# Kernel tuning notes

Measured on AMD Instinct MI355X. Metric: run time of the kernel, lower is better.

Reference implementation:

```python
import jax, jax.numpy as jnp
import numpy as np

B, T, D, U = 64, 512, 1024, 1024


def hard_sigmoid(x):
    # keras hard_sigmoid: clip(0.2*x + 0.5, 0, 1)
    return jnp.clip(0.2 * x + 0.5, 0.0, 1.0)


def setup_inputs() -> dict:
    key = jax.random.key(0)
    ks = jax.random.split(key, 6)
    x = jax.random.normal(ks[0], (B, T, D), jnp.float32)
    # glorot-ish scaled params
    kernel = jax.random.normal(ks[1], (D, 4 * U), jnp.float32) * (1.0 / np.sqrt(D).astype(np.float32))
    recurrent_kernel = jax.random.normal(ks[2], (U, 4 * U), jnp.float32) * (1.0 / np.sqrt(U).astype(np.float32))
    peephole_kernel = jax.random.normal(ks[3], (U, 3 * U), jnp.float32) * (1.0 / np.sqrt(U).astype(np.float32))
    projection_kernel = jax.random.normal(ks[4], (U, U), jnp.float32) * (1.0 / np.sqrt(U).astype(np.float32))
    # unit_forget_bias: [zeros(U), ones(U), zeros(2U)] for (i, f, c, o)
    bias = jnp.concatenate([jnp.zeros((U,), jnp.float32), jnp.ones((U,), jnp.float32), jnp.zeros((2 * U,), jnp.float32)])
    h0 = jnp.zeros((B, U), jnp.float32)
    c0 = jnp.zeros((B, U), jnp.float32)
    return {"x": x, "h0": h0, "c0": c0, "kernel": kernel, "recurrent_kernel": recurrent_kernel,
            "peephole_kernel": peephole_kernel, "projection_kernel": projection_kernel, "bias": bias}


def reference(x, h0, c0, kernel, recurrent_kernel, peephole_kernel, projection_kernel, bias):
    U_ = h0.shape[-1]
    Pi = peephole_kernel[:, :U_]
    Pf = peephole_kernel[:, U_:2 * U_]
    Po = peephole_kernel[:, 2 * U_:3 * U_]

    def step(carry, x_t):
        h, c = carry
        # fused gate pre-activations: [B, 4U]
        z = x_t @ kernel + h @ recurrent_kernel + bias
        zi, zf, zc, zo = jnp.split(z, 4, axis=-1)
        i = hard_sigmoid(zi + c @ Pi)            # input gate w/ peephole on c_{t-1}
        f = hard_sigmoid(zf + c @ Pf)            # forget gate w/ peephole on c_{t-1}
        c_new = f * c + i * jnp.tanh(zc)
        o = hard_sigmoid(zo + c_new @ Po)        # output gate w/ peephole on c_t
        # residual LSTM: project tanh(c_t), add residual input, gate by o
        h_new = o * (jnp.tanh(c_new) @ projection_kernel + x_t)
        return (h_new, c_new), h_new

    xs = jnp.swapaxes(x, 0, 1)  # [T, B, D]
    (_, _), hs = jax.lax.scan(step, (h0, c0), xs)
    return jnp.swapaxes(hs, 0, 1)  # [B, T, U]
```

## Files before the change

### kernel.cpp

```cpp
#include <hip/hip_runtime.h>
#include <cstdint>
#include <cstddef>

#define NB 64
#define NT 512
#define ND 1024
#define NU 1024

typedef short s16x8 __attribute__((ext_vector_type(8)));
typedef float f32x4 __attribute__((ext_vector_type(4)));
typedef unsigned int u32x2 __attribute__((ext_vector_type(2)));
typedef unsigned int u32x4 __attribute__((ext_vector_type(4)));
typedef unsigned short u16;

__device__ __forceinline__ u16 f2bf(float f) {
  unsigned int u = __float_as_uint(f);
  u += 0x7fffu + ((u >> 16) & 1u);
  return (u16)(u >> 16);
}
__device__ __forceinline__ float bf2f(u16 s) {
  return __uint_as_float(((unsigned int)s) << 16);
}
__device__ __forceinline__ float hsig(float x) {
  return fminf(fmaxf(0.2f * x + 0.5f, 0.0f), 1.0f);
}
__device__ __forceinline__ float ftanh(float x) {
  float e = __expf(2.0f * x);
  return 1.0f - 2.0f / (e + 1.0f);
}
__device__ __forceinline__ f32x4 mfma16(s16x8 a, s16x8 b, f32x4 c) {
  return __builtin_amdgcn_mfma_f32_16x16x32_bf16(a, b, c, 0, 0, 0);
}

__device__ __forceinline__ void atomic_swap_u32(unsigned int* p, unsigned int v) {
  asm volatile("global_atomic_swap %0, %1, off" :: "v"(p), "v"(v) : "memory");
}
__device__ __forceinline__ void atomic_swap_u64(unsigned int* p, u32x2 v) {
  asm volatile("global_atomic_swap_x2 %0, %1, off" :: "v"(p), "v"(v) : "memory");
}

template <int STAGED>
__device__ __forceinline__ void ldx4(s16x8& d, const u16* a) {
  if constexpr (STAGED)
    asm volatile("global_load_dwordx4 %0, %1, off" : "=v"(d) : "v"(a));
  else
    asm volatile("global_load_dwordx4 %0, %1, off sc0 sc1" : "=v"(d) : "v"(a));
}

#define WAIT_VM0() do { \
    asm volatile("s_waitcnt vmcnt(0)" ::: "memory"); \
    __builtin_amdgcn_sched_barrier(0); \
  } while (0)
#define WAIT_VM(N) do { \
    asm volatile("s_waitcnt vmcnt(" #N ")" ::: "memory"); \
    __builtin_amdgcn_sched_barrier(0); \
  } while (0)

__global__ __launch_bounds__(256) void wt_cvt(const float* __restrict__ W,
                                              u16* __restrict__ Wt) {
  __shared__ u16 T[64][65];
  const int tid = threadIdx.x;
  const int k0 = (blockIdx.x & 15) * 64;
  const int n0 = (blockIdx.x >> 4) * 64;
  const int r = tid >> 2, c4 = (tid & 3) * 16;
  {
    const float* src = W + (size_t)(k0 + r) * 4096 + n0 + c4;
#pragma unroll
    for (int j = 0; j < 4; ++j) {
      float4 v = ((const float4*)src)[j];
      T[r][c4 + j * 4 + 0] = f2bf(v.x); T[r][c4 + j * 4 + 1] = f2bf(v.y);
      T[r][c4 + j * 4 + 2] = f2bf(v.z); T[r][c4 + j * 4 + 3] = f2bf(v.w);
    }
  }
  __syncthreads();
  {
    u16 tmp[16];
#pragma unroll
    for (int i = 0; i < 16; ++i) tmp[i] = T[c4 + i][r];
    u16* dst = Wt + (size_t)(n0 + r) * 1024 + k0 + c4;
    *(s16x8*)dst = *(s16x8*)tmp;
    *(s16x8*)(dst + 8) = *(s16x8*)(tmp + 8);
  }
}

template <int WT>
__global__ __launch_bounds__(256) void xw_gemm(const float* __restrict__ X,
                                               const float* __restrict__ W,
                                               const u16* __restrict__ Wt,
                                               u16* __restrict__ XW) {
  __shared__ u16 Al[128][72];
  __shared__ u16 Bl[128][72];
  const int tid = threadIdx.x;
  const int lane = tid & 63;
  const int wv = tid >> 6;
  const int m0 = (blockIdx.x >> 5) * 128;
  const int n0 = (blockIdx.x & 31) * 128;
  f32x4 acc[4][4];
#pragma unroll
  for (int i = 0; i < 4; ++i)
#pragma unroll
    for (int j = 0; j < 4; ++j) acc[i][j] = (f32x4){0.f, 0.f, 0.f, 0.f};

  for (int kt = 0; kt < 1024; kt += 64) {
    {
      const int r = tid >> 1, hh = (tid & 1) * 32;
      const float* src = X + (size_t)(m0 + r) * 1024 + kt + hh;
      u16* dst = &Al[r][hh];
      if constexpr (WT) {
#pragma unroll
        for (int j = 0; j < 4; ++j) {
          float4 v0 = ((const float4*)src)[2 * j];
          float4 v1 = ((const float4*)src)[2 * j + 1];
          u32x4 q;
          q[0] = ((unsigned)f2bf(v0.y) << 16) | f2bf(v0.x);
          q[1] = ((unsigned)f2bf(v0.w) << 16) | f2bf(v0.z);
          q[2] = ((unsigned)f2bf(v1.y) << 16) | f2bf(v1.x);
          q[3] = ((unsigned)f2bf(v1.w) << 16) | f2bf(v1.z);
          *(u32x4*)(dst + j * 8) = q;
        }
      } else {
#pragma unroll
        for (int j = 0; j < 8; ++j) {
          float4 v = ((const float4*)src)[j];
          dst[j * 4 + 0] = f2bf(v.x); dst[j * 4 + 1] = f2bf(v.y);
          dst[j * 4 + 2] = f2bf(v.z); dst[j * 4 + 3] = f2bf(v.w);
        }
      }
    }
    if constexpr (WT) {
      const int n = tid >> 1, kh = (tid & 1) * 32;
      const u16* src = Wt + (size_t)(n0 + n) * 1024 + kt + kh;
      u16* dst = &Bl[n][kh];
#pragma unroll
      for (int j = 0; j < 4; ++j)
        *(s16x8*)(dst + j * 8) = *(const s16x8*)(src + j * 8);
    } else {
      const int kr = tid >> 2, q = (tid & 3) * 32;
      const float* src = W + (size_t)(kt + kr) * 4096 + n0 + q;
#pragma unroll
      for (int j = 0; j < 8; ++j) {
        float4 v = ((const float4*)src)[j];
        const int n = q + j * 4;
        Bl[n + 0][kr] = f2bf(v.x); Bl[n + 1][kr] = f2bf(v.y);
        Bl[n + 2][kr] = f2bf(v.z); Bl[n + 3][kr] = f2bf(v.w);
      }
    }
    __syncthreads();
    const int wm = (wv >> 1) * 64, wn = (wv & 1) * 64;
    const int row = lane & 15, kq = (lane >> 4) * 8;
#pragma unroll
    for (int ks = 0; ks < 2; ++ks) {
      s16x8 af[4], bq[4];
#pragma unroll
      for (int i = 0; i < 4; ++i) af[i] = *(const s16x8*)&Al[wm + i * 16 + row][ks * 32 + kq];
#pragma unroll
      for (int j = 0; j < 4; ++j) bq[j] = *(const s16x8*)&Bl[wn + j * 16 + row][ks * 32 + kq];
#pragma unroll
      for (int i = 0; i < 4; ++i)
#pragma unroll
        for (int j = 0; j < 4; ++j) acc[i][j] = mfma16(af[i], bq[j], acc[i][j]);
    }
    __syncthreads();
  }
  const int wm = (wv >> 1) * 64, wn = (wv & 1) * 64;
  const int col16 = lane & 15, rq = (lane >> 4) * 4;
#pragma unroll
  for (int i = 0; i < 4; ++i)
#pragma unroll
    for (int j = 0; j < 4; ++j)
#pragma unroll
      for (int q = 0; q < 4; ++q) {
        const int m = m0 + wm + i * 16 + rq + q;
        const int n = n0 + wn + j * 16 + col16;
        const int t = m & 511, b = m >> 9;
        const int g = n >> 10, uu = n & 1023;
        const int ugrp = uu >> 4, ul2 = uu & 15;
        XW[(((size_t)ugrp * 512 + t) * 64 + b) * 64 + ul2 * 4 + g] = f2bf(acc[i][j][q]);
      }
}

__global__ void init_comm(const float* __restrict__ h0, const float* __restrict__ c0,
                          u16* hini, u16* cini) {
  const int i = blockIdx.x * 256 + threadIdx.x;
  hini[i] = f2bf(h0[i]);
  cini[i] = f2bf(c0[i]);
}

__device__ __forceinline__ void gbar_arrive(unsigned int* flags, int bid, int tid,
                                            unsigned int ep) {
  __syncthreads();
  if (tid == 0) atomic_swap_u32(flags + bid * 16, ep);
}
__device__ __forceinline__ void gbar_poll(unsigned int* flags, int rq, int tid,
                                          unsigned int ep) {
  unsigned int* f = flags + ((((tid & 63) << 2) | rq) * 16);
  for (;;) {
    unsigned int v;
    asm volatile("global_load_dword %0, %1, off sc0 sc1\n\ts_waitcnt vmcnt(0)"
                 : "=v"(v) : "v"(f) : "memory");
    if (v >= ep) break;
    __builtin_amdgcn_s_sleep(1);
  }
  __builtin_amdgcn_sched_barrier(0);
}

#define WLDS_B   (64 * 1032 * 2)
#define ZOFF     WLDS_B
#define POFF     (ZOFF + 16 * 68 * 4)
#define OOFF     (POFF + 16 * 36 * 4)
#define SMEM_B   (OOFF + 16 * 36 * 4)
#define STEP_E   65536

template <int STAGED>
__global__ __launch_bounds__(256, 1) void lstm_loop(
    const float* __restrict__ rec, const float* __restrict__ peep,
    const float* __restrict__ projw, const float* __restrict__ bias,
    const float* __restrict__ x, const u16* __restrict__ xw,
    float* __restrict__ out,
    u16* hini, u16* cini, u16* cb0, u16* cb1, u16* thsg,
    u16* hst, u16* cst, u16* thst,
    unsigned int* flags, const float* __restrict__ c0) {
  extern __shared__ char smem[];
  u16 (*wlds)[1032] = (u16(*)[1032])smem;
  float (*zlds)[68] = (float(*)[68])(smem + ZOFF);
  float (*plds)[36] = (float(*)[36])(smem + POFF);
  float (*olds)[36] = (float(*)[36])(smem + OOFF);

  const int tid = threadIdx.x;
  const int lane = tid & 63;
  const int wv = tid >> 6;
  const int bid = blockIdx.x;
  const int ugrp = bid >> 2;
  const int rq = bid & 3;
  const int row0 = rq * 16;
  const int u0 = ugrp * 16;
  const int fcol = lane & 15;
  const int kofs = (lane >> 4) * 8;

  for (int g = 0; g < 8; ++g) {
    const int c = g * 8 + (tid & 3) * 2;
    const int scol = (c >> 4) * 1024 + u0 + (c & 15);
#pragma unroll 4
    for (int p = 0; p < 16; ++p) {
      const int k = p * 64 + (tid >> 2);
      float2 v = *(const float2*)(rec + (size_t)k * 4096 + scol);
      wlds[c][k] = f2bf(v.x);
      wlds[c + 1][k] = f2bf(v.y);
    }
  }
  __syncthreads();
  s16x8 breg[32];
#pragma unroll
  for (int kt = 0; kt < 32; ++kt)
    breg[kt] = *(const s16x8*)&wlds[wv * 16 + fcol][kt * 32 + kofs];
  __syncthreads();
  for (int g = 0; g < 8; ++g) {
    const int c = g * 8 + (tid & 3) * 2;
    const float* sp; int stride, scol;
    if (c < 48) { sp = peep;  stride = 3072; scol = (c >> 4) * 1024 + u0 + (c & 15); }
    else        { sp = projw; stride = 1024; scol = u0 + (c & 15); }
#pragma unroll 4
    for (int p = 0; p < 16; ++p) {
      const int k = p * 64 + (tid >> 2);
      float2 v = *(const float2*)(sp + (size_t)k * stride + scol);
      wlds[c][k] = f2bf(v.x);
      wlds[c + 1][k] = f2bf(v.y);
    }
  }

  const int r = tid >> 4;
  const int ul = tid & 15;
  const int brow = row0 + r;
  const int u = u0 + ul;
  const float b_i = bias[u], b_f = bias[1024 + u], b_c = bias[2048 + u], b_o = bias[3072 + u];
  float cstv = c0[brow * 1024 + u];

  u32x2 xwp;
  float xp;
  {
    const u16* xr0 = xw + (((size_t)ugrp * 512 + 0) * 64 + brow) * 64 + ul * 4;
    asm volatile("global_load_dwordx2 %0, %1, off" : "=v"(xwp) : "v"(xr0));
    const float* xs0 = x + (size_t)brow * (512 * 1024) + u;
    asm volatile("global_load_dword %0, %1, off" : "=v"(xp) : "v"(xs0));
  }
  __syncthreads();

  for (int t = 0; t < NT; ++t) {
    const size_t xo = (size_t)brow * (512 * 1024) + (size_t)t * 1024 + u;
    float zo_reg, xres, hv;

    const u16 *hsrc, *cpsrc, *csrc, *thsrc; u16 *cpub, *thpub, *hpub;
    if constexpr (STAGED) {
      hsrc  = t ? (hst + (size_t)(t - 1) * STEP_E) : hini;
      cpsrc = t ? (cst + (size_t)(t - 1) * STEP_E) : cini;
      cpub  = cst + (size_t)t * STEP_E;   csrc = cpub;
      thpub = thst + (size_t)t * STEP_E;  thsrc = thpub;
      hpub  = hst + (size_t)t * STEP_E;
    } else {
      hsrc = hini; hpub = hini;
      cpub = (t & 1) ? cb1 : cb0; csrc = cpub;
      cpsrc = (t == 0) ? cini : ((t & 1) ? cb0 : cb1);
      thpub = thsg; thsrc = thsg;
    }

    s16x8 av[32];
    if (wv < 2) {
      s16x8 cv[32];
      {
        const u16* ap = cpsrc + (size_t)(row0 + fcol) * 1024 + kofs;
#pragma unroll
        for (int kt = 0; kt < 32; ++kt) ldx4<STAGED>(cv[kt], ap + kt * 32);
      }
      gbar_poll(flags, rq, tid, 2 * (unsigned)t);
      f32x4 accP = {0.f, 0.f, 0.f, 0.f};
      const u16* bp = &wlds[wv * 16 + fcol][kofs];
#pragma unroll
      for (int kt = 0; kt < 32; ++kt)
        accP = mfma16(cv[kt], *(const s16x8*)(bp + kt * 32), accP);
      {
        const u16* ap = hsrc + (size_t)(row0 + fcol) * 1024 + kofs;
#pragma unroll
        for (int kt = 0; kt < 32; ++kt) ldx4<STAGED>(av[kt], ap + kt * 32);
      }
      WAIT_VM0();
      f32x4 accZ = {0.f, 0.f, 0.f, 0.f};
#pragma unroll
      for (int kt = 0; kt < 32; ++kt) accZ = mfma16(av[kt], breg[kt], accZ);
      const int srow = (lane >> 4) * 4;
#pragma unroll
      for (int q = 0; q < 4; ++q) {
        zlds[srow + q][wv * 16 + fcol] = accZ[q];
        plds[srow + q][wv * 16 + fcol] = accP[q];
      }
    } else {
      gbar_poll(flags, rq, tid, 2 * (unsigned)t);
      {
        const u16* ap = hsrc + (size_t)(row0 + fcol) * 1024 + kofs;
#pragma unroll
        for (int kt = 0; kt < 32; ++kt) ldx4<STAGED>(av[kt], ap + kt * 32);
      }
      WAIT_VM0();
      f32x4 accZ = {0.f, 0.f, 0.f, 0.f};
#pragma unroll
      for (int kt = 0; kt < 32; ++kt) accZ = mfma16(av[kt], breg[kt], accZ);
      const int srow = (lane >> 4) * 4;
#pragma unroll
      for (int q = 0; q < 4; ++q) zlds[srow + q][wv * 16 + fcol] = accZ[q];
    }
    __syncthreads();
    {
      const float xw_i = bf2f((u16)(xwp[0] & 0xffffu));
      const float xw_f = bf2f((u16)(xwp[0] >> 16));
      const float xw_c = bf2f((u16)(xwp[1] & 0xffffu));
      const float xw_o = bf2f((u16)(xwp[1] >> 16));
      xres = xp;
      const float zi = zlds[r][ul]      + xw_i + b_i + plds[r][ul];
      const float zf = zlds[r][16 + ul] + xw_f + b_f + plds[r][16 + ul];
      const float zc = zlds[r][32 + ul] + xw_c + b_c;
      zo_reg         = zlds[r][48 + ul] + xw_o + b_o;
      const float ig = hsig(zi), fg = hsig(zf);
      cstv = fg * cstv + ig * ftanh(zc);
      const float th = ftanh(cstv);
      const unsigned int cb = f2bf(cstv), tb = f2bf(th);
      const unsigned int cp = ((unsigned)__shfl_xor((int)cb, 1) << 16) | cb;
      const unsigned int tp = ((unsigned)__shfl_xor((int)tb, 1) << 16) | tb;
      const unsigned int cp2 = (unsigned)__shfl_xor((int)cp, 2);
      const unsigned int tp2 = (unsigned)__shfl_xor((int)tp, 2);
      if ((ul & 3) == 0) {
        u32x2 cq; cq[0] = cp; cq[1] = cp2;
        u32x2 tq; tq[0] = tp; tq[1] = tp2;
        atomic_swap_u64((unsigned int*)(cpub + brow * 1024 + u), cq);
        atomic_swap_u64((unsigned int*)(thpub + brow * 1024 + u), tq);
      }
    }
    WAIT_VM0();
    gbar_arrive(flags, bid, tid, 2 * t + 1);

    if (!STAGED || wv >= 2) gbar_poll(flags, rq, tid, 2 * t + 1);
    if (wv >= 2) {
      const u16* ap = ((wv == 2) ? csrc : thsrc)
                      + (size_t)(row0 + fcol) * 1024 + kofs;
#pragma unroll
      for (int kt = 0; kt < 32; ++kt) ldx4<STAGED>(av[kt], ap + kt * 32);
      WAIT_VM0();
      f32x4 acc = {0.f, 0.f, 0.f, 0.f};
      const u16* bp = &wlds[wv * 16 + fcol][kofs];
#pragma unroll
      for (int kt = 0; kt < 32; ++kt)
        acc = mfma16(av[kt], *(const s16x8*)(bp + kt * 32), acc);
      const int srow = (lane >> 4) * 4;
#pragma unroll
      for (int q = 0; q < 4; ++q) olds[srow + q][(wv - 2) * 16 + fcol] = acc[q];
    }
    __syncthreads();
    {
      const float og = hsig(zo_reg + olds[r][ul]);
      const float pv = olds[r][16 + ul] + xres;
      hv = og * pv;
      const unsigned int hb = f2bf(hv);
      const unsigned int hp = ((unsigned)__shfl_xor((int)hb, 1) << 16) | hb;
      const unsigned int hp2 = (unsigned)__shfl_xor((int)hp, 2);
      if ((ul & 3) == 0) {
        u32x2 hq; hq[0] = hp; hq[1] = hp2;
        atomic_swap_u64((unsigned int*)(hpub + brow * 1024 + u), hq);
      }
      const int tn = (t + 1 < NT) ? (t + 1) : t;
      const u16* xrn = xw + (((size_t)ugrp * 512 + tn) * 64 + brow) * 64 + ul * 4;
      asm volatile("global_load_dwordx2 %0, %1, off" : "=v"(xwp) : "v"(xrn));
      const float* xsn = x + (size_t)brow * (512 * 1024) + (size_t)tn * 1024 + u;
      asm volatile("global_load_dword %0, %1, off" : "=v"(xp) : "v"(xsn));
      asm volatile("global_store_dword %0, %1, off" :: "v"(out + xo), "v"(hv) : "memory");
      WAIT_VM(3);
    }
    gbar_arrive(flags, bid, tid, 2 * t + 2);
  }
}

extern "C" void kernel_launch(void* const* d_in, const int* in_sizes, int n_in,
                              void* d_out, int out_size, void* d_ws, size_t ws_size,
                              hipStream_t stream) {
  const float* x    = (const float*)d_in[0];
  const float* h0   = (const float*)d_in[1];
  const float* c0   = (const float*)d_in[2];
  const float* W    = (const float*)d_in[3];
  const float* R    = (const float*)d_in[4];
  const float* P    = (const float*)d_in[5];
  const float* PRJ  = (const float*)d_in[6];
  const float* bias = (const float*)d_in[7];
  float* out = (float*)d_out;
  char* ws = (char*)d_ws;

  const size_t XW_BYTES = (size_t)32768 * 4096 * 2;
  size_t off = XW_BYTES;
  u16* xw   = (u16*)ws;
  u16* hini = (u16*)(ws + off); off += 131072;
  u16* cini = (u16*)(ws + off); off += 131072;
  u16* cb0  = (u16*)(ws + off); off += 131072;
  u16* cb1  = (u16*)(ws + off); off += 131072;
  u16* thsg = (u16*)(ws + off); off += 131072;
  unsigned int* flags = (unsigned int*)(ws + off); off += 16384;
  const size_t base_need = off;
  u16* hst = (u16*)(ws + off);  off += (size_t)NT * 131072;
  u16* cst = (u16*)(ws + off);  off += (size_t)NT * 131072;
  u16* thst = (u16*)(ws + off); off += (size_t)NT * 131072;
  const size_t staged_need = off;
  u16* Wt = (u16*)(ws + off); off += (size_t)4096 * 1024 * 2;
  const size_t wt_need = off;
  if (ws_size < base_need) return;
  const int staged = (ws_size >= staged_need) ? 1 : 0;
  const int wt = (ws_size >= wt_need) ? 1 : 0;

  (void)hipFuncSetAttribute(reinterpret_cast<const void*>(&lstm_loop<1>),
                            hipFuncAttributeMaxDynamicSharedMemorySize, 160 * 1024);
  (void)hipFuncSetAttribute(reinterpret_cast<const void*>(&lstm_loop<0>),
                            hipFuncAttributeMaxDynamicSharedMemorySize, 160 * 1024);

  hipMemsetAsync(flags, 0, 16384, stream);
  hipLaunchKernelGGL(init_comm, dim3(256), dim3(256), 0, stream, h0, c0, hini, cini);
  if (wt) {
    hipLaunchKernelGGL(wt_cvt, dim3(1024), dim3(256), 0, stream, W, Wt);
    hipLaunchKernelGGL((xw_gemm<1>), dim3(8192), dim3(256), 0, stream, x, W, Wt, xw);
  } else {
    hipLaunchKernelGGL((xw_gemm<0>), dim3(8192), dim3(256), 0, stream, x, W, Wt, xw);
  }

  void* args[17];
  args[0] = (void*)&R;     args[1] = (void*)&P;     args[2] = (void*)&PRJ;
  args[3] = (void*)&bias;  args[4] = (void*)&x;     args[5] = (void*)&xw;
  args[6] = (void*)&out;   args[7] = (void*)&hini;  args[8] = (void*)&cini;
  args[9] = (void*)&cb0;   args[10] = (void*)&cb1;  args[11] = (void*)&thsg;
  args[12] = (void*)&hst;  args[13] = (void*)&cst;  args[14] = (void*)&thst;
  args[15] = (void*)&flags; args[16] = (void*)&c0;

  const void* fn = staged ? (const void*)&lstm_loop<1> : (const void*)&lstm_loop<0>;
  hipError_t e = hipLaunchCooperativeKernel(fn, dim3(256), dim3(256),
                                            args, (unsigned int)SMEM_B, stream);
  if (e != hipSuccess) {
    if (staged)
      hipLaunchKernelGGL((lstm_loop<1>), dim3(256), dim3(256), SMEM_B, stream,
                         R, P, PRJ, bias, x, xw, out, hini, cini, cb0, cb1, thsg,
                         hst, cst, thst, flags, c0);
    else
      hipLaunchKernelGGL((lstm_loop<0>), dim3(256), dim3(256), SMEM_B, stream,
                         R, P, PRJ, bias, x, xw, out, hini, cini, cb0, cb1, thsg,
                         hst, cst, thst, flags, c0);
  }
}
```

Measured before the change: 7.169 ms.

## Poll barrier flags per k-slice group and overlap loads with partial arrivals

Replaces the all-flags barrier poll with per-16-lane-group polling. Each quarter of the K dimension is loaded and multiplied as soon as the producer blocks owning that slice have arrived, so waiting overlaps with MFMA work instead of stalling on the slowest producer. The peephole c-matmul now runs fully before the h-poll, and wave 0-1 no longer polls the second epoch in the non-staged path. The risk is more poll round-trips per step, shorter load batches with a full vmcnt wait per slice, and possible ordering bugs if a group's flag coverage does not match its k-slice.

Result: slower. 7.542 ms (+5.2%).

```diff
diff --git a/kernel.cpp b/kernel.cpp
--- a/kernel.cpp
+++ b/kernel.cpp
@@ -191,18 +191,62 @@
   __syncthreads();
   if (tid == 0) atomic_swap_u32(flags + bid * 16, ep);
 }
-__device__ __forceinline__ void gbar_poll(unsigned int* flags, int rq, int tid,
-                                          unsigned int ep) {
-  unsigned int* f = flags + ((((tid & 63) << 2) | rq) * 16);
-  for (;;) {
-    unsigned int v;
-    asm volatile("global_load_dword %0, %1, off sc0 sc1\n\ts_waitcnt vmcnt(0)"
-                 : "=v"(v) : "v"(f) : "memory");
-    if (v >= ep) break;
-    __builtin_amdgcn_s_sleep(1);
-  }
-  __builtin_amdgcn_sched_barrier(0);
-}
+
+#define POLL_GRP(S, EP) \
+  do { \
+    if ((lane >> 4) == (S)) { \
+      unsigned int pv_; \
+      for (;;) { \
+        asm volatile("global_load_dword %0, %1, off sc0 sc1\n\ts_waitcnt vmcnt(0)" \
+                     : "=v"(pv_) : "v"(myflag) : "memory"); \
+        if (pv_ >= (EP)) break; \
+        __builtin_amdgcn_s_sleep(1); \
+      } \
+    } \
+    __builtin_amdgcn_sched_barrier(0); \
+  } while (0)
+
+#define ZCONS(S) do { \
+    s16x8 a0_, a1_, a2_, a3_, a4_, a5_, a6_, a7_; \
+    ldx4<STAGED>(a0_, ap + ((S) * 8 + 0) * 32); \
+    ldx4<STAGED>(a1_, ap + ((S) * 8 + 1) * 32); \
+    ldx4<STAGED>(a2_, ap + ((S) * 8 + 2) * 32); \
+    ldx4<STAGED>(a3_, ap + ((S) * 8 + 3) * 32); \
+    ldx4<STAGED>(a4_, ap + ((S) * 8 + 4) * 32); \
+    ldx4<STAGED>(a5_, ap + ((S) * 8 + 5) * 32); \
+    ldx4<STAGED>(a6_, ap + ((S) * 8 + 6) * 32); \
+    ldx4<STAGED>(a7_, ap + ((S) * 8 + 7) * 32); \
+    WAIT_VM0(); \
+    accZ = mfma16(a0_, breg[(S) * 8 + 0], accZ); \
+    accZ = mfma16(a1_, breg[(S) * 8 + 1], accZ); \
+    accZ = mfma16(a2_, breg[(S) * 8 + 2], accZ); \
+    accZ = mfma16(a3_, breg[(S) * 8 + 3], accZ); \
+    accZ = mfma16(a4_, breg[(S) * 8 + 4], accZ); \
+    accZ = mfma16(a5_, breg[(S) * 8 + 5], accZ); \
+    accZ = mfma16(a6_, breg[(S) * 8 + 6], accZ); \
+    accZ = mfma16(a7_, breg[(S) * 8 + 7], accZ); \
+  } while (0)
+
+#define OCONS(S) do { \
+    s16x8 a0_, a1_, a2_, a3_, a4_, a5_, a6_, a7_; \
+    ldx4<STAGED>(a0_, ap2 + ((S) * 8 + 0) * 32); \
+    ldx4<STAGED>(a1_, ap2 + ((S) * 8 + 1) * 32); \
+    ldx4<STAGED>(a2_, ap2 + ((S) * 8 + 2) * 32); \
+    ldx4<STAGED>(a3_, ap2 + ((S) * 8 + 3) * 32); \
+    ldx4<STAGED>(a4_, ap2 + ((S) * 8 + 4) * 32); \
+    ldx4<STAGED>(a5_, ap2 + ((S) * 8 + 5) * 32); \
+    ldx4<STAGED>(a6_, ap2 + ((S) * 8 + 6) * 32); \
+    ldx4<STAGED>(a7_, ap2 + ((S) * 8 + 7) * 32); \
+    WAIT_VM0(); \
+    accO = mfma16(a0_, *(const s16x8*)(bp2 + ((S) * 8 + 0) * 32), accO); \
+    accO = mfma16(a1_, *(const s16x8*)(bp2 + ((S) * 8 + 1) * 32), accO); \
+    accO = mfma16(a2_, *(const s16x8*)(bp2 + ((S) * 8 + 2) * 32), accO); \
+    accO = mfma16(a3_, *(const s16x8*)(bp2 + ((S) * 8 + 3) * 32), accO); \
+    accO = mfma16(a4_, *(const s16x8*)(bp2 + ((S) * 8 + 4) * 32), accO); \
+    accO = mfma16(a5_, *(const s16x8*)(bp2 + ((S) * 8 + 5) * 32), accO); \
+    accO = mfma16(a6_, *(const s16x8*)(bp2 + ((S) * 8 + 6) * 32), accO); \
+    accO = mfma16(a7_, *(const s16x8*)(bp2 + ((S) * 8 + 7) * 32), accO); \
+  } while (0)
 
 #define WLDS_B   (64 * 1032 * 2)
 #define ZOFF     WLDS_B
@@ -275,6 +319,8 @@
   const float b_i = bias[u], b_f = bias[1024 + u], b_c = bias[2048 + u], b_o = bias[3072 + u];
   float cstv = c0[brow * 1024 + u];
 
+  unsigned int* myflag = flags + (((lane << 2) | rq) * 16);
+
   u32x2 xwp;
   float xp;
   {
@@ -303,46 +349,29 @@
       thpub = thsg; thsrc = thsg;
     }
 
-    s16x8 av[32];
     if (wv < 2) {
       s16x8 cv[32];
-      {
-        const u16* ap = cpsrc + (size_t)(row0 + fcol) * 1024 + kofs;
-#pragma unroll
-        for (int kt = 0; kt < 32; ++kt) ldx4<STAGED>(cv[kt], ap + kt * 32);
-      }
-      gbar_poll(flags, rq, tid, 2 * (unsigned)t);
+      const u16* cap = cpsrc + (size_t)(row0 + fcol) * 1024 + kofs;
+#pragma unroll
+      for (int kt = 0; kt < 32; ++kt) ldx4<STAGED>(cv[kt], cap + kt * 32);
+      WAIT_VM0();
       f32x4 accP = {0.f, 0.f, 0.f, 0.f};
-      const u16* bp = &wlds[wv * 16 + fcol][kofs];
+      const u16* pbp = &wlds[wv * 16 + fcol][kofs];
 #pragma unroll
       for (int kt = 0; kt < 32; ++kt)
-        accP = mfma16(cv[kt], *(const s16x8*)(bp + kt * 32), accP);
-      {
-        const u16* ap = hsrc + (size_t)(row0 + fcol) * 1024 + kofs;
-#pragma unroll
-        for (int kt = 0; kt < 32; ++kt) ldx4<STAGED>(av[kt], ap + kt * 32);
-      }
-      WAIT_VM0();
+        accP = mfma16(cv[kt], *(const s16x8*)(pbp + kt * 32), accP);
+      const int srow = (lane >> 4) * 4;
+#pragma unroll
+      for (int q = 0; q < 4; ++q) plds[srow + q][wv * 16 + fcol] = accP[q];
+    }
+    {
+      const unsigned int ep1 = 2 * (unsigned)t;
+      const u16* ap = hsrc + (size_t)(row0 + fcol) * 1024 + kofs;
       f32x4 accZ = {0.f, 0.f, 0.f, 0.f};
-#pragma unroll
-      for (int kt = 0; kt < 32; ++kt) accZ = mfma16(av[kt], breg[kt], accZ);
-      const int srow = (lane >> 4) * 4;
-#pragma unroll
-      for (int q = 0; q < 4; ++q) {
-        zlds[srow + q][wv * 16 + fcol] = accZ[q];
-        plds[srow + q][wv * 16 + fcol] = accP[q];
-      }
-    } else {
-      gbar_poll(flags, rq, tid, 2 * (unsigned)t);
-      {
-        const u16* ap = hsrc + (size_t)(row0 + fcol) * 1024 + kofs;
-#pragma unroll
-        for (int kt = 0; kt < 32; ++kt) ldx4<STAGED>(av[kt], ap + kt * 32);
-      }
-      WAIT_VM0();
-      f32x4 accZ = {0.f, 0.f, 0.f, 0.f};
-#pragma unroll
-      for (int kt = 0; kt < 32; ++kt) accZ = mfma16(av[kt], breg[kt], accZ);
+      POLL_GRP(0, ep1); ZCONS(0);
+      POLL_GRP(1, ep1); ZCONS(1);
+      POLL_GRP(2, ep1); ZCONS(2);
+      POLL_GRP(3, ep1); ZCONS(3);
       const int srow = (lane >> 4) * 4;
 #pragma unroll
       for (int q = 0; q < 4; ++q) zlds[srow + q][wv * 16 + fcol] = accZ[q];
@@ -376,21 +405,19 @@
     WAIT_VM0();
     gbar_arrive(flags, bid, tid, 2 * t + 1);
 
-    if (!STAGED || wv >= 2) gbar_poll(flags, rq, tid, 2 * t + 1);
     if (wv >= 2) {
-      const u16* ap = ((wv == 2) ? csrc : thsrc)
-                      + (size_t)(row0 + fcol) * 1024 + kofs;
-#pragma unroll
-      for (int kt = 0; kt < 32; ++kt) ldx4<STAGED>(av[kt], ap + kt * 32);
-      WAIT_VM0();
-      f32x4 acc = {0.f, 0.f, 0.f, 0.f};
-      const u16* bp = &wlds[wv * 16 + fcol][kofs];
-#pragma unroll
-      for (int kt = 0; kt < 32; ++kt)
-        acc = mfma16(av[kt], *(const s16x8*)(bp + kt * 32), acc);
+      const unsigned int ep2 = 2 * (unsigned)t + 1;
+      const u16* ap2 = ((wv == 2) ? csrc : thsrc)
+                       + (size_t)(row0 + fcol) * 1024 + kofs;
+      const u16* bp2 = &wlds[wv * 16 + fcol][kofs];
+      f32x4 accO = {0.f, 0.f, 0.f, 0.f};
+      POLL_GRP(0, ep2); OCONS(0);
+      POLL_GRP(1, ep2); OCONS(1);
+      POLL_GRP(2, ep2); OCONS(2);
+      POLL_GRP(3, ep2); OCONS(3);
       const int srow = (lane >> 4) * 4;
 #pragma unroll
-      for (int q = 0; q < 4; ++q) olds[srow + q][(wv - 2) * 16 + fcol] = acc[q];
+      for (int q = 0; q < 4; ++q) olds[srow + q][(wv - 2) * 16 + fcol] = accO[q];
     }
     __syncthreads();
     {
```

## Replace flag-based grid barriers with epoch-tagged data words polled directly

Applied to the files above, without the earlier changes.

Removes the global flag barriers between timesteps. Each published h, c and tanh(c) element now goes into a 32-bit word whose upper 16 bits carry the step epoch, in double-buffered slots. Consumers spin-load the data itself until every word carries the expected epoch, then pack the bf16 halves for MFMA. This drops the barrier round trips and the separate flag polling, but it doubles the communication bytes, adds unpack ALU work, and relies on per-word atomic visibility for correctness.

Result: slower. 13.36 ms (+86.3%).

```diff
diff --git a/kernel.cpp b/kernel.cpp
--- a/kernel.cpp
+++ b/kernel.cpp
@@ -32,27 +32,15 @@
   return __builtin_amdgcn_mfma_f32_16x16x32_bf16(a, b, c, 0, 0, 0);
 }
 
-__device__ __forceinline__ void atomic_swap_u32(unsigned int* p, unsigned int v) {
-  asm volatile("global_atomic_swap %0, %1, off" :: "v"(p), "v"(v) : "memory");
-}
 __device__ __forceinline__ void atomic_swap_u64(unsigned int* p, u32x2 v) {
   asm volatile("global_atomic_swap_x2 %0, %1, off" :: "v"(p), "v"(v) : "memory");
 }
-
-template <int STAGED>
-__device__ __forceinline__ void ldx4(s16x8& d, const u16* a) {
-  if constexpr (STAGED)
-    asm volatile("global_load_dwordx4 %0, %1, off" : "=v"(d) : "v"(a));
-  else
-    asm volatile("global_load_dwordx4 %0, %1, off sc0 sc1" : "=v"(d) : "v"(a));
+__device__ __forceinline__ void ldw4(u32x4& d, const unsigned int* a) {
+  asm volatile("global_load_dwordx4 %0, %1, off sc0 sc1" : "=v"(d) : "v"(a));
 }
 
 #define WAIT_VM0() do { \
     asm volatile("s_waitcnt vmcnt(0)" ::: "memory"); \
-    __builtin_amdgcn_sched_barrier(0); \
-  } while (0)
-#define WAIT_VM(N) do { \
-    asm volatile("s_waitcnt vmcnt(" #N ")" ::: "memory"); \
     __builtin_amdgcn_sched_barrier(0); \
   } while (0)
 
@@ -180,28 +168,41 @@
 }
 
 __global__ void init_comm(const float* __restrict__ h0, const float* __restrict__ c0,
-                          u16* hini, u16* cini) {
+                          unsigned int* h2, unsigned int* c2) {
   const int i = blockIdx.x * 256 + threadIdx.x;
-  hini[i] = f2bf(h0[i]);
-  cini[i] = f2bf(c0[i]);
-}
-
-__device__ __forceinline__ void gbar_arrive(unsigned int* flags, int bid, int tid,
-                                            unsigned int ep) {
-  __syncthreads();
-  if (tid == 0) atomic_swap_u32(flags + bid * 16, ep);
-}
-__device__ __forceinline__ void gbar_poll(unsigned int* flags, int rq, int tid,
-                                          unsigned int ep) {
-  unsigned int* f = flags + ((((tid & 63) << 2) | rq) * 16);
-  for (;;) {
-    unsigned int v;
-    asm volatile("global_load_dword %0, %1, off sc0 sc1\n\ts_waitcnt vmcnt(0)"
-                 : "=v"(v) : "v"(f) : "memory");
-    if (v >= ep) break;
-    __builtin_amdgcn_s_sleep(1);
-  }
-  __builtin_amdgcn_sched_barrier(0);
+  h2[65536 + i] = (unsigned int)f2bf(h0[i]);
+  c2[65536 + i] = (unsigned int)f2bf(c0[i]);
+}
+
+__device__ __forceinline__ f32x4 consume_lds(const unsigned int* ap, const u16* bp,
+                                             unsigned int ep, f32x4 acc) {
+#pragma unroll
+  for (int ch = 0; ch < 4; ++ch) {
+    u32x4 w[16];
+    for (;;) {
+#pragma unroll
+      for (int j = 0; j < 16; ++j)
+        ldw4(w[j], ap + ch * 256 + (j >> 1) * 32 + (j & 1) * 4);
+      WAIT_VM0();
+      bool ok = true;
+#pragma unroll
+      for (int j = 0; j < 16; ++j)
+#pragma unroll
+        for (int e = 0; e < 4; ++e) ok = ok && ((w[j][e] >> 16) == ep);
+      if (__all(ok)) break;
+      __builtin_amdgcn_s_sleep(1);
+    }
+#pragma unroll
+    for (int i = 0; i < 8; ++i) {
+      u32x4 p;
+      p[0] = (w[2 * i][1] << 16) | (w[2 * i][0] & 0xffffu);
+      p[1] = (w[2 * i][3] << 16) | (w[2 * i][2] & 0xffffu);
+      p[2] = (w[2 * i + 1][1] << 16) | (w[2 * i + 1][0] & 0xffffu);
+      p[3] = (w[2 * i + 1][3] << 16) | (w[2 * i + 1][2] & 0xffffu);
+      acc = mfma16(*(const s16x8*)&p, *(const s16x8*)(bp + (ch * 8 + i) * 32), acc);
+    }
+  }
+  return acc;
 }
 
 #define WLDS_B   (64 * 1032 * 2)
@@ -209,17 +210,15 @@
 #define POFF     (ZOFF + 16 * 68 * 4)
 #define OOFF     (POFF + 16 * 36 * 4)
 #define SMEM_B   (OOFF + 16 * 36 * 4)
-#define STEP_E   65536
-
-template <int STAGED>
+#define SLOT_W   65536u
+
 __global__ __launch_bounds__(256, 1) void lstm_loop(
     const float* __restrict__ rec, const float* __restrict__ peep,
     const float* __restrict__ projw, const float* __restrict__ bias,
     const float* __restrict__ x, const u16* __restrict__ xw,
     float* __restrict__ out,
-    u16* hini, u16* cini, u16* cb0, u16* cb1, u16* thsg,
-    u16* hst, u16* cst, u16* thst,
-    unsigned int* flags, const float* __restrict__ c0) {
+    unsigned int* h2, unsigned int* c2, unsigned int* th2,
+    const float* __restrict__ c0) {
   extern __shared__ char smem[];
   u16 (*wlds)[1032] = (u16(*)[1032])smem;
   float (*zlds)[68] = (float(*)[68])(smem + ZOFF);
@@ -285,64 +284,53 @@
   }
   __syncthreads();
 
+  const size_t lrow = (size_t)(row0 + fcol) * 1024 + kofs;
+  const size_t prow = (size_t)brow * 1024 + u;
+
   for (int t = 0; t < NT; ++t) {
     const size_t xo = (size_t)brow * (512 * 1024) + (size_t)t * 1024 + u;
+    const unsigned int sPrev = ((unsigned)(t + 1) & 1u) * SLOT_W;
+    const unsigned int sCur  = ((unsigned)t & 1u) * SLOT_W;
+    const unsigned int epPrev = (unsigned)t;
+    const unsigned int epCur  = (unsigned)(t + 1);
     float zo_reg, xres, hv;
 
-    const u16 *hsrc, *cpsrc, *csrc, *thsrc; u16 *cpub, *thpub, *hpub;
-    if constexpr (STAGED) {
-      hsrc  = t ? (hst + (size_t)(t - 1) * STEP_E) : hini;
-      cpsrc = t ? (cst + (size_t)(t - 1) * STEP_E) : cini;
-      cpub  = cst + (size_t)t * STEP_E;   csrc = cpub;
-      thpub = thst + (size_t)t * STEP_E;  thsrc = thpub;
-      hpub  = hst + (size_t)t * STEP_E;
-    } else {
-      hsrc = hini; hpub = hini;
-      cpub = (t & 1) ? cb1 : cb0; csrc = cpub;
-      cpsrc = (t == 0) ? cini : ((t & 1) ? cb0 : cb1);
-      thpub = thsg; thsrc = thsg;
-    }
-
-    s16x8 av[32];
     if (wv < 2) {
-      s16x8 cv[32];
-      {
-        const u16* ap = cpsrc + (size_t)(row0 + fcol) * 1024 + kofs;
-#pragma unroll
-        for (int kt = 0; kt < 32; ++kt) ldx4<STAGED>(cv[kt], ap + kt * 32);
-      }
-      gbar_poll(flags, rq, tid, 2 * (unsigned)t);
-      f32x4 accP = {0.f, 0.f, 0.f, 0.f};
-      const u16* bp = &wlds[wv * 16 + fcol][kofs];
-#pragma unroll
-      for (int kt = 0; kt < 32; ++kt)
-        accP = mfma16(cv[kt], *(const s16x8*)(bp + kt * 32), accP);
-      {
-        const u16* ap = hsrc + (size_t)(row0 + fcol) * 1024 + kofs;
-#pragma unroll
-        for (int kt = 0; kt < 32; ++kt) ldx4<STAGED>(av[kt], ap + kt * 32);
-      }
-      WAIT_VM0();
+      f32x4 accP = consume_lds(c2 + sPrev + lrow, &wlds[wv * 16 + fcol][kofs],
+                               epPrev, (f32x4){0.f, 0.f, 0.f, 0.f});
+      const int srow = (lane >> 4) * 4;
+#pragma unroll
+      for (int q = 0; q < 4; ++q) plds[srow + q][wv * 16 + fcol] = accP[q];
+    }
+    {
+      const unsigned int* hp = h2 + sPrev + lrow;
       f32x4 accZ = {0.f, 0.f, 0.f, 0.f};
 #pragma unroll
-      for (int kt = 0; kt < 32; ++kt) accZ = mfma16(av[kt], breg[kt], accZ);
-      const int srow = (lane >> 4) * 4;
-#pragma unroll
-      for (int q = 0; q < 4; ++q) {
-        zlds[srow + q][wv * 16 + fcol] = accZ[q];
-        plds[srow + q][wv * 16 + fcol] = accP[q];
-      }
-    } else {
-      gbar_poll(flags, rq, tid, 2 * (unsigned)t);
-      {
-        const u16* ap = hsrc + (size_t)(row0 + fcol) * 1024 + kofs;
-#pragma unroll
-        for (int kt = 0; kt < 32; ++kt) ldx4<STAGED>(av[kt], ap + kt * 32);
-      }
-      WAIT_VM0();
-      f32x4 accZ = {0.f, 0.f, 0.f, 0.f};
-#pragma unroll
-      for (int kt = 0; kt < 32; ++kt) accZ = mfma16(av[kt], breg[kt], accZ);
+      for (int ch = 0; ch < 4; ++ch) {
+        u32x4 w[16];
+        for (;;) {
+#pragma unroll
+          for (int j = 0; j < 16; ++j)
+            ldw4(w[j], hp + ch * 256 + (j >> 1) * 32 + (j & 1) * 4);
+          WAIT_VM0();
+          bool ok = true;
+#pragma unroll
+          for (int j = 0; j < 16; ++j)
+#pragma unroll
+            for (int e = 0; e < 4; ++e) ok = ok && ((w[j][e] >> 16) == epPrev);
+          if (__all(ok)) break;
+          __builtin_amdgcn_s_sleep(1);
+        }
+#pragma unroll
+        for (int i = 0; i < 8; ++i) {
+          u32x4 p;
+          p[0] = (w[2 * i][1] << 16) | (w[2 * i][0] & 0xffffu);
+          p[1] = (w[2 * i][3] << 16) | (w[2 * i][2] & 0xffffu);
+          p[2] = (w[2 * i + 1][1] << 16) | (w[2 * i + 1][0] & 0xffffu);
+          p[3] = (w[2 * i + 1][3] << 16) | (w[2 * i + 1][2] & 0xffffu);
+          accZ = mfma16(*(const s16x8*)&p, breg[ch * 8 + i], accZ);
+        }
+      }
       const int srow = (lane >> 4) * 4;
 #pragma unroll
       for (int q = 0; q < 4; ++q) zlds[srow + q][wv * 16 + fcol] = accZ[q];
@@ -361,48 +349,37 @@
       const float ig = hsig(zi), fg = hsig(zf);
       cstv = fg * cstv + ig * ftanh(zc);
       const float th = ftanh(cstv);
-      const unsigned int cb = f2bf(cstv), tb = f2bf(th);
-      const unsigned int cp = ((unsigned)__shfl_xor((int)cb, 1) << 16) | cb;
-      const unsigned int tp = ((unsigned)__shfl_xor((int)tb, 1) << 16) | tb;
-      const unsigned int cp2 = (unsigned)__shfl_xor((int)cp, 2);
-      const unsigned int tp2 = (unsigned)__shfl_xor((int)tp, 2);
-      if ((ul & 3) == 0) {
-        u32x2 cq; cq[0] = cp; cq[1] = cp2;
-        u32x2 tq; tq[0] = tp; tq[1] = tp2;
-        atomic_swap_u64((unsigned int*)(cpub + brow * 1024 + u), cq);
-        atomic_swap_u64((unsigned int*)(thpub + brow * 1024 + u), tq);
-      }
-    }
-    WAIT_VM0();
-    gbar_arrive(flags, bid, tid, 2 * t + 1);
-
-    if (!STAGED || wv >= 2) gbar_poll(flags, rq, tid, 2 * t + 1);
+      const unsigned int epw = epCur << 16;
+      const unsigned int wc = epw | f2bf(cstv);
+      const unsigned int wt_ = epw | f2bf(th);
+      const unsigned int wc1 = (unsigned)__shfl_xor((int)wc, 1);
+      const unsigned int wt1 = (unsigned)__shfl_xor((int)wt_, 1);
+      if ((ul & 1) == 0) {
+        u32x2 cq; cq[0] = wc;  cq[1] = wc1;
+        u32x2 tq; tq[0] = wt_; tq[1] = wt1;
+        atomic_swap_u64(c2 + sCur + prow, cq);
+        atomic_swap_u64(th2 + sCur + prow, tq);
+      }
+    }
+
     if (wv >= 2) {
-      const u16* ap = ((wv == 2) ? csrc : thsrc)
-                      + (size_t)(row0 + fcol) * 1024 + kofs;
-#pragma unroll
-      for (int kt = 0; kt < 32; ++kt) ldx4<STAGED>(av[kt], ap + kt * 32);
-      WAIT_VM0();
-      f32x4 acc = {0.f, 0.f, 0.f, 0.f};
-      const u16* bp = &wlds[wv * 16 + fcol][kofs];
-#pragma unroll
-      for (int kt = 0; kt < 32; ++kt)
-        acc = mfma16(av[kt], *(const s16x8*)(bp + kt * 32), acc);
+      const unsigned int* ap2 = ((wv == 2) ? c2 : th2) + sCur + lrow;
+      f32x4 accO = consume_lds(ap2, &wlds[wv * 16 + fcol][kofs],
+                               epCur, (f32x4){0.f, 0.f, 0.f, 0.f});
       const int srow = (lane >> 4) * 4;
 #pragma unroll
-      for (int q = 0; q < 4; ++q) olds[srow + q][(wv - 2) * 16 + fcol] = acc[q];
+      for (int q = 0; q < 4; ++q) olds[srow + q][(wv - 2) * 16 + fcol] = accO[q];
     }
     __syncthreads();
     {
       const float og = hsig(zo_reg + olds[r][ul]);
       const float pv = olds[r][16 + ul] + xres;
       hv = og * pv;
-      const unsigned int hb = f2bf(hv);
-      const unsigned int hp = ((unsigned)__shfl_xor((int)hb, 1) << 16) | hb;
-      const unsigned int hp2 = (unsigned)__shfl_xor((int)hp, 2);
-      if ((ul & 3) == 0) {
-        u32x2 hq; hq[0] = hp; hq[1] = hp2;
-        atomic_swap_u64((unsigned int*)(hpub + brow * 1024 + u), hq);
+      const unsigned int hw = (epCur << 16) | f2bf(hv);
+      const unsigned int hw1 = (unsigned)__shfl_xor((int)hw, 1);
+      if ((ul & 1) == 0) {
+        u32x2 hq; hq[0] = hw; hq[1] = hw1;
+        atomic_swap_u64(h2 + sCur + prow, hq);
       }
       const int tn = (t + 1 < NT) ? (t + 1) : t;
       const u16* xrn = xw + (((size_t)ugrp * 512 + tn) * 64 + brow) * 64 + ul * 4;
@@ -410,10 +387,9 @@
       const float* xsn = x + (size_t)brow * (512 * 1024) + (size_t)tn * 1024 + u;
       asm volatile("global_load_dword %0, %1, off" : "=v"(xp) : "v"(xsn));
       asm volatile("global_store_dword %0, %1, off" :: "v"(out + xo), "v"(hv) : "memory");
-      WAIT_VM(3);
-    }
-    gbar_arrive(flags, bid, tid, 2 * t + 2);
-  }
+    }
+  }
+  WAIT_VM0();
 }
 
 extern "C" void kernel_launch(void* const* d_in, const int* in_sizes, int n_in,
@@ -432,31 +408,20 @@
 
   const size_t XW_BYTES = (size_t)32768 * 4096 * 2;
   size_t off = XW_BYTES;
-  u16* xw   = (u16*)ws;
-  u16* hini = (u16*)(ws + off); off += 131072;
-  u16* cini = (u16*)(ws + off); off += 131072;
-  u16* cb0  = (u16*)(ws + off); off += 131072;
-  u16* cb1  = (u16*)(ws + off); off += 131072;
-  u16* thsg = (u16*)(ws + off); off += 131072;
-  unsigned int* flags = (unsigned int*)(ws + off); off += 16384;
+  u16* xw = (u16*)ws;
+  unsigned int* h2  = (unsigned int*)(ws + off); off += 2 * 65536 * 4;
+  unsigned int* c2  = (unsigned int*)(ws + off); off += 2 * 65536 * 4;
+  unsigned int* th2 = (unsigned int*)(ws + off); off += 2 * 65536 * 4;
   const size_t base_need = off;
-  u16* hst = (u16*)(ws + off);  off += (size_t)NT * 131072;
-  u16* cst = (u16*)(ws + off);  off += (size_t)NT * 131072;
-  u16* thst = (u16*)(ws + off); off += (size_t)NT * 131072;
-  const size_t staged_need = off;
   u16* Wt = (u16*)(ws + off); off += (size_t)4096 * 1024 * 2;
   const size_t wt_need = off;
   if (ws_size < base_need) return;
-  const int staged = (ws_size >= staged_need) ? 1 : 0;
   const int wt = (ws_size >= wt_need) ? 1 : 0;
 
-  (void)hipFuncSetAttribute(reinterpret_cast<const void*>(&lstm_loop<1>),
+  (void)hipFuncSetAttribute(reinterpret_cast<const void*>(&lstm_loop),
                             hipFuncAttributeMaxDynamicSharedMemorySize, 160 * 1024);
-  (void)hipFuncSetAttribute(reinterpret_cast<const void*>(&lstm_loop<0>),
-                            hipFuncAttributeMaxDynamicSharedMemorySize, 160 * 1024);
-
-  hipMemsetAsync(flags, 0, 16384, stream);
-  hipLaunchKernelGGL(init_comm, dim3(256), dim3(256), 0, stream, h0, c0, hini, cini);
+
+  hipLaunchKernelGGL(init_comm, dim3(256), dim3(256), 0, stream, h0, c0, h2, c2);
   if (wt) {
     hipLaunchKernelGGL(wt_cvt, dim3(1024), dim3(256), 0, stream, W, Wt);
     hipLaunchKernelGGL((xw_gemm<1>), dim3(8192), dim3(256), 0, stream, x, W, Wt, xw);
@@ -464,25 +429,16 @@
     hipLaunchKernelGGL((xw_gemm<0>), dim3(8192), dim3(256), 0, stream, x, W, Wt, xw);
   }
 
-  void* args[17];
-  args[0] = (void*)&R;     args[1] = (void*)&P;     args[2] = (void*)&PRJ;
-  args[3] = (void*)&bias;  args[4] = (void*)&x;     args[5] = (void*)&xw;
-  args[6] = (void*)&out;   args[7] = (void*)&hini;  args[8] = (void*)&cini;
-  args[9] = (void*)&cb0;   args[10] = (void*)&cb1;  args[11] = (void*)&thsg;
-  args[12] = (void*)&hst;  args[13] = (void*)&cst;  args[14] = (void*)&thst;
-  args[15] = (void*)&flags; args[16] = (void*)&c0;
-
-  const void* fn = staged ? (const void*)&lstm_loop<1> : (const void*)&lstm_loop<0>;
-  hipError_t e = hipLaunchCooperativeKernel(fn, dim3(256), dim3(256),
+  void* args[11];
+  args[0] = (void*)&R;    args[1] = (void*)&P;   args[2] = (void*)&PRJ;
+  args[3] = (void*)&bias; args[4] = (void*)&x;   args[5] = (void*)&xw;
+  args[6] = (void*)&out;  args[7] = (void*)&h2;  args[8] = (void*)&c2;
+  args[9] = (void*)&th2;  args[10] = (void*)&c0;
+
+  hipError_t e = hipLaunchCooperativeKernel((const void*)&lstm_loop, dim3(256), dim3(256),
                                             args, (unsigned int)SMEM_B, stream);
   if (e != hipSuccess) {
-    if (staged)
-      hipLaunchKernelGGL((lstm_loop<1>), dim3(256), dim3(256), SMEM_B, stream,
-                         R, P, PRJ, bias, x, xw, out, hini, cini, cb0, cb1, thsg,
-                         hst, cst, thst, flags, c0);
-    else
-      hipLaunchKernelGGL((lstm_loop<0>), dim3(256), dim3(256), SMEM_B, stream,
-                         R, P, PRJ, bias, x, xw, out, hini, cini, cb0, cb1, thsg,
-                         hst, cst, thst, flags, c0);
-  }
-}
+    hipLaunchKernelGGL(lstm_loop, dim3(256), dim3(256), SMEM_B, stream,
+                       R, P, PRJ, bias, x, xw, out, h2, c2, th2, c0);
+  }
+}
```
